# Kernel optimization log

Hardware: AMD Instinct MI355X
Metric: run time of the kernel (lower is better)

## Reference

```python
import jax, jax.numpy as jnp
import numpy as np

K = 5          # number of neighbors (init kwarg k)
EPS = 1e-7     # init kwarg eps
_D2_MIN = 1e-12  # clamp squared distances so sqrt is grad-safe on the diagonal


def _cdist(A):
    # Euclidean pairwise distances, [N, N]
    sq = jnp.sum(A * A, axis=1)
    d2 = sq[:, None] + sq[None, :] - 2.0 * (A @ A.T)
    return jnp.sqrt(jnp.maximum(d2, _D2_MIN))


def setup_inputs() -> dict:
    key = jax.random.key(0)
    k1, k2 = jax.random.split(key)
    X = jax.random.normal(k1, (8192, 512), dtype=jnp.float32)
    Z = jax.random.normal(k2, (8192, 128), dtype=jnp.float32)
    return {"X": X, "Z": Z}


def reference(X, Z):
    # 0.98-quantile of row norms (torch.quantile default = linear interpolation)
    normA1 = jnp.quantile(jnp.sqrt(jnp.sum(X ** 2, axis=1)), 0.98)
    normA2 = jnp.quantile(jnp.sqrt(jnp.sum(Z ** 2, axis=1)), 0.98)

    # --- neighbor mask + LID on X ---
    x_dist = (_cdist(X) + EPS) / normA1                      # [N, N]
    neg_vals, idx = jax.lax.top_k(-x_dist, K + 1)            # k+1 smallest, ascending
    values = -neg_vals[:, 1:]                                # drop self, [N, K]
    nn_mask = idx[:, 1:]                                     # neighbor indices, [N, K]
    lid_X = jnp.sum(jnp.log10(values) - jnp.log10(values[:, -1:]), axis=1)  # [N]

    # --- gather same neighbors in Z-space ---
    z_dist = (_cdist(Z) + EPS) / normA2                      # [N, N]
    extracted = jnp.take_along_axis(z_dist, nn_mask, axis=1)  # [N, K]
    norm_v = jnp.max(extracted, axis=1, keepdims=True)        # [N, 1]
    lid_Z = jnp.sum(jnp.log10(extracted) - jnp.log10(norm_v), axis=1)  # [N]

    N = X.shape[0]
    diff = K / (lid_X + EPS) - K / (lid_Z + EPS)
    return jnp.sum(jnp.square(diff)) / (N * K * K)
```

## Files before the change

kernel.cpp:

```cpp
#include <hip/hip_runtime.h>
#include <hip/hip_bf16.h>
#include <math.h>


#define NROWS 8192
#define DX 512
#define DZ 128
#define KNN 5
#define NSTRIP 4
#define SSPAN (NROWS / NSTRIP)
#define BM 128
#define BN 256
#define NJT (SSPAN / BN)
#define NCAND (NSTRIP * KNN)
#define QSCALE 30.0f

typedef int i32x4 __attribute__((ext_vector_type(4)));
typedef int i32x16 __attribute__((ext_vector_type(16)));

__device__ __forceinline__ bool ilexless(int d1, int i1, int d2, int i2) {
  return (d1 < d2) || (d1 == d2 && i1 < i2);
}
__device__ __forceinline__ bool flexless(float d1, int i1, float d2, int i2) {
  return (d1 < d2) || (d1 == d2 && i1 < i2);
}

__device__ __forceinline__ void ins5k(int k, int* md) {
  if (k >= md[4]) return;
  int nk = k;
#pragma unroll
  for (int p = 0; p < 5; ++p) {
    const bool sw = nk < md[p];
    const int tk = sw ? md[p] : nk;
    md[p] = sw ? nk : md[p];
    nk = tk;
  }
}
__device__ __forceinline__ void ins6k(int k, int* md) {
  if (k >= md[5]) return;
  int nk = k;
#pragma unroll
  for (int p = 0; p < 6; ++p) {
    const bool sw = nk < md[p];
    const int tk = sw ? md[p] : nk;
    md[p] = sw ? nk : md[p];
    nk = tk;
  }
}
__device__ __forceinline__ void ins8i(int d, int i, int* md, int* mi) {
  if (!ilexless(d, i, md[7], mi[7])) return;
  int nd = d, ni = i;
#pragma unroll
  for (int p = 0; p < 8; ++p) {
    const bool sw = ilexless(nd, ni, md[p], mi[p]);
    const int td = sw ? md[p] : nd; const int ti = sw ? mi[p] : ni;
    md[p] = sw ? nd : md[p]; mi[p] = sw ? ni : mi[p];
    nd = td; ni = ti;
  }
}
__device__ __forceinline__ void ins5f(float d, int i, float* md, int* mi) {
  if (!flexless(d, i, md[4], mi[4])) return;
  float nd = d; int ni = i;
#pragma unroll
  for (int p = 0; p < 5; ++p) {
    const bool sw = flexless(nd, ni, md[p], mi[p]);
    const float td = sw ? md[p] : nd; const int ti = sw ? mi[p] : ni;
    md[p] = sw ? nd : md[p]; mi[p] = sw ? ni : mi[p];
    nd = td; ni = ti;
  }
}

__device__ __forceinline__ void gload_lds16(const void* g, void* l) {
  __builtin_amdgcn_global_load_lds((const __attribute__((address_space(1))) void*)g,
                                   (__attribute__((address_space(3))) void*)l,
                                   16, 0, 0);
}

__global__ __launch_bounds__(256) void prep_kernel(const float* __restrict__ X,
                                                   const float* __restrict__ Z,
                                                   signed char* __restrict__ Xq,
                                                   float* __restrict__ sqx,
                                                   int* __restrict__ sqq,
                                                   float* __restrict__ sqz) {
  const int b = blockIdx.x;
  const int w = threadIdx.x >> 6;
  const int lane = threadIdx.x & 63;
  if (b < NROWS / 4) {
    const int row = (b << 2) + w;
    const float* p = X + (size_t)row * DX + lane * 8;
    const float4 v0 = *(const float4*)(p);
    const float4 v1 = *(const float4*)(p + 4);
    float xs[8] = {v0.x, v0.y, v0.z, v0.w, v1.x, v1.y, v1.z, v1.w};
    float s = 0.f;
    int q[8];
    int si = 0;
#pragma unroll
    for (int j = 0; j < 8; ++j) {
      s = fmaf(xs[j], xs[j], s);
      q[j] = (int)rintf(fminf(fmaxf(xs[j] * QSCALE, -127.f), 127.f));
      si += q[j] * q[j];
    }
    const int b0 = (q[0] & 255) | ((q[1] & 255) << 8) | ((q[2] & 255) << 16) | ((q[3] & 255) << 24);
    const int b1 = (q[4] & 255) | ((q[5] & 255) << 8) | ((q[6] & 255) << 16) | ((q[7] & 255) << 24);
    *(int2*)(Xq + (size_t)row * DX + lane * 8) = make_int2(b0, b1);
#pragma unroll
    for (int off = 32; off > 0; off >>= 1) {
      s += __shfl_down(s, off, 64);
      si += __shfl_down(si, off, 64);
    }
    if (lane == 0) { sqx[row] = s; sqq[row] = si; }
  } else {
    const int row = ((b - NROWS / 4) << 2) + w;
    const float* p = Z + (size_t)row * DZ;
    const float a = p[lane];
    const float c = p[64 + lane];
    float s = fmaf(a, a, c * c);
#pragma unroll
    for (int off = 32; off > 0; off >>= 1) s += __shfl_down(s, off, 64);
    if (lane == 0) sqz[row] = s;
  }
}

__global__ __launch_bounds__(1024) void stats_kernel(const int* __restrict__ sqq,
                                                     float* __restrict__ stats) {
  __shared__ double sw[16], sw2[16];
  const int t = threadIdx.x;
  double s = 0.0, s2 = 0.0;
  for (int i = t; i < NROWS; i += 1024) {
    const double v = (double)sqq[i];
    s += v; s2 += v * v;
  }
#pragma unroll
  for (int off = 32; off > 0; off >>= 1) {
    s += __shfl_down(s, off, 64);
    s2 += __shfl_down(s2, off, 64);
  }
  if ((t & 63) == 0) { sw[t >> 6] = s; sw2[t >> 6] = s2; }
  __syncthreads();
  if (t < 16) {
    double v = sw[t], v2 = sw2[t];
#pragma unroll
    for (int off = 8; off > 0; off >>= 1) {
      v += __shfl_down(v, off, 64);
      v2 += __shfl_down(v2, off, 64);
    }
    if (t == 0) {
      const double mu = v / (double)NROWS;
      stats[0] = (float)mu;
      stats[1] = (float)(v2 / (double)NROWS - mu * mu);
    }
  }
}

__global__ __launch_bounds__(1024, 1) void knn_i8_kernel(const signed char* __restrict__ Xq,
                                                         const int* __restrict__ sqq,
                                                         const float* __restrict__ stats,
                                                         int* __restrict__ cand_i,
                                                         int* __restrict__ cand_m) {
  extern __shared__ __align__(16) char lds[];
  char* ldsA = lds;
  char* ldsBb = lds + 65536;
  int* qs = (int*)(lds + 114688);

  const int bid = blockIdx.x;
  const int strip = bid & 3;
  const int rowchunk = bid >> 2;
  const int I0 = rowchunk * BM;
  const int J0 = strip * SSPAN;

  const int t = threadIdx.x;
  const int w = t >> 6;
  const int lane = t & 63;
  const int l31 = lane & 31, lh5 = lane >> 5;
  const int cq = w & 3, rh = w >> 2;

  const float mu = stats[0];
  const float var = stats[1];
  const int lr = (rh << 5) + l31;
  const int tau = (int)(mu - 2.2f * sqrtf(var + (mu * 0.0078125f) * (float)sqq[I0 + lr]));
  const int taubase = tau - 262144;

  const char* Aaddr = ldsA + (lh5 << 11) + (lr << 4);
  const int bcol = ((cq << 6) + l31) << 4;
  const char* Ba0 = ldsBb + (lh5 << 12) + bcol;
  const char* Ba1 = Ba0 + 16384;
  const char* Ba2 = Ba0 + 32768;
  char* Da0 = ldsBb + ((w >> 2) << 12) + ((w & 3) << 10);
  char* Da1 = Da0 + 16384;
  char* Da2 = Da0 + 32768;
  const signed char* sj = Xq + (size_t)(J0 + ((w & 3) << 6) + lane) * DX + ((w >> 2) << 4);
  const int* qw = qs + (cq << 6) + (lh5 << 2);
  int colj = J0 + (cq << 6) + (lh5 << 2);

#pragma unroll
  for (int i = 0; i < 4; ++i) {
    const int idx = (w << 2) + i;
    const int g = idx >> 1, half = idx & 1;
    gload_lds16(Xq + (size_t)(I0 + half * 64 + lane) * DX + (g << 4),
                ldsA + g * 2048 + half * 1024);
  }
  if (w < 8)
    gload_lds16((const char*)(sqq + J0) + (w << 10) + (lane << 4),
                (char*)qs + (w << 10));
  gload_lds16(sj, Da0);
  gload_lds16(sj + 64, Da1);

  const i32x16 z16 = {0, 0, 0, 0, 0, 0, 0, 0, 0, 0, 0, 0, 0, 0, 0, 0};
  i32x16 acc[2];
  int md6[6];
#pragma unroll
  for (int q = 0; q < 6; ++q) md6[q] = 0x7fffffff;

  for (int jt = 0; jt < NJT; ++jt) {
    const signed char* sj2 = sj + BN * DX;
#pragma unroll
    for (int kb = 0; kb < 8; ++kb) {
      if (kb < 7 || jt < NJT - 1) {
        asm volatile("s_waitcnt vmcnt(1)" ::: "memory");
      } else {
        asm volatile("s_waitcnt vmcnt(0)" ::: "memory");
      }
      __builtin_amdgcn_s_barrier();
      __builtin_amdgcn_sched_barrier(0);
      char* D = (kb % 3 == 1) ? Da0 : (kb % 3 == 2) ? Da1 : Da2;
      if (kb <= 5) {
        gload_lds16(sj + (kb + 2) * 64, D);
      } else if (jt < NJT - 1) {
        gload_lds16(sj2 + (kb - 6) * 64, D);
      }
      if (kb == 0) { acc[0] = z16; acc[1] = z16; }
      const char* B = (kb % 3 == 0) ? Ba0 : (kb % 3 == 1) ? Ba1 : Ba2;
#pragma unroll
      for (int ktl = 0; ktl < 2; ++ktl) {
        const i32x4 ap0 = *(const i32x4*)(B + ktl * 8192);
        const i32x4 ap1 = *(const i32x4*)(B + ktl * 8192 + 512);
        const i32x4 bp = *(const i32x4*)(Aaddr + kb * 8192 + ktl * 4096);
        acc[0] = __builtin_amdgcn_mfma_i32_32x32x32_i8(ap0, bp, acc[0], 0, 0, 0);
        acc[1] = __builtin_amdgcn_mfma_i32_32x32x32_i8(ap1, bp, acc[1], 0, 0, 0);
      }
      if (kb == 7) {
#pragma unroll
        for (int n = 0; n < 2; ++n) {
          const i32x4 q0 = *(const i32x4*)(qw + n * 32);
          const i32x4 q1 = *(const i32x4*)(qw + n * 32 + 8);
          const i32x4 q2 = *(const i32x4*)(qw + n * 32 + 16);
          const i32x4 q3 = *(const i32x4*)(qw + n * 32 + 24);
#pragma unroll
          for (int reg = 0; reg < 16; ++reg) {
            const int qv = (reg < 4) ? q0[reg & 3] : (reg < 8) ? q1[reg & 3]
                         : (reg < 12) ? q2[reg & 3] : q3[reg & 3];
            const int d = qv - 2 * acc[n][reg];
            if (d < tau) {
              const int cconst = (reg & 3) + ((reg >> 2) << 3);
              const int col = colj + n * 32 + cconst;
              const int v = max(d - taubase, 0);
              ins6k((v << 13) | col, md6);
            }
          }
        }
      }
    }
    { const char* tmp = Ba2; Ba2 = Ba1; Ba1 = Ba0; Ba0 = tmp; }
    { char* tmp = Da2; Da2 = Da1; Da1 = Da0; Da0 = tmp; }
    sj = sj2; qw += BN; colj += BN;
  }

  __syncthreads();

  int* pm = (int*)ldsBb;
  {
    const int sub = (cq << 1) | lh5;
#pragma unroll
    for (int q = 0; q < 6; ++q) pm[(lr * 8 + sub) * 6 + q] = md6[q];
  }
  __syncthreads();
  if (t < BM) {
    int md[5];
#pragma unroll
    for (int q = 0; q < 5; ++q) md[q] = 0x7fffffff;
    const int rgg = I0 + t;
    for (int c = 0; c < 8; ++c)
#pragma unroll
      for (int q = 0; q < 6; ++q) {
        const int key = pm[(t * 8 + c) * 6 + q];
        if ((key & 8191) != rgg) ins5k(key, md);
      }
    const size_t base = (size_t)(I0 + t) * NCAND + strip * KNN;
#pragma unroll
    for (int q = 0; q < 5; ++q) {
      cand_m[base + q] = md[q];
      cand_i[base + q] = (md[q] == 0x7fffffff) ? 0x7fffffff : (md[q] & 8191);
    }
  }
}

__global__ __launch_bounds__(256) void rerank_kernel(const float* __restrict__ X,
                                                     const float* __restrict__ Z,
                                                     const float* __restrict__ sqx,
                                                     const float* __restrict__ sqz,
                                                     const int* __restrict__ cand_i,
                                                     const int* __restrict__ cand_m,
                                                     float* __restrict__ row_out) {
  __shared__ float xrow[4][DX];
  const int w = threadIdx.x >> 6;
  const int lane = threadIdx.x & 63;
  const int row = (blockIdx.x << 2) + w;

  const float* xp = X + (size_t)row * DX + lane * 8;
  *(float4*)&xrow[w][lane * 8] = *(const float4*)(xp);
  *(float4*)&xrow[w][lane * 8 + 4] = *(const float4*)(xp + 4);

  int cm = 0x7fffffff, ci = 0x7fffffff;
  if (lane < NCAND) {
    cm = cand_m[(size_t)row * NCAND + lane];
    ci = cand_i[(size_t)row * NCAND + lane];
  }
  __syncthreads();

  int m8[8], i8v[8];
#pragma unroll
  for (int q = 0; q < 8; ++q) { m8[q] = 0x7fffffff; i8v[q] = 0x7fffffff; }
#pragma unroll
  for (int c = 0; c < NCAND; ++c) {
    const int dm = __shfl(cm, c, 64);
    const int di = __shfl(ci, c, 64);
    ins8i(dm, di, m8, i8v);
  }

  const int cgrp = lane >> 3, sgi = lane & 7;
  int j = (cgrp == 0) ? i8v[0] : (cgrp == 1) ? i8v[1] : (cgrp == 2) ? i8v[2] :
          (cgrp == 3) ? i8v[3] : (cgrp == 4) ? i8v[4] : (cgrp == 5) ? i8v[5] :
          (cgrp == 6) ? i8v[6] : i8v[7];
  if ((unsigned)j >= NROWS) j = 0;
  const float* yp = X + (size_t)j * DX + sgi * 64;
  const float* xq_ = &xrow[w][sgi * 64];
  float dot = 0.f;
#pragma unroll 8
  for (int k = 0; k < 64; k += 4) {
    const float4 xv = *(const float4*)(xq_ + k);
    const float4 yv = *(const float4*)(yp + k);
    dot = fmaf(xv.x, yv.x, dot);
    dot = fmaf(xv.y, yv.y, dot);
    dot = fmaf(xv.z, yv.z, dot);
    dot = fmaf(xv.w, yv.w, dot);
  }
  dot += __shfl_xor(dot, 1, 64);
  dot += __shfl_xor(dot, 2, 64);
  dot += __shfl_xor(dot, 4, 64);
  const float d2 = sqx[row] + sqx[j] - 2.f * dot;

  float fd[5]; int fi[5];
#pragma unroll
  for (int q = 0; q < 5; ++q) { fd[q] = INFINITY; fi[q] = 0x7fffffff; }
#pragma unroll
  for (int cc = 0; cc < 8; ++cc) {
    const float dd = __shfl(d2, cc * 8, 64);
    if (lane == 0) ins5f(dd, i8v[cc], fd, fi);
  }
  float lidX = 0.f;
  if (lane == 0) {
    const float v4 = sqrtf(fmaxf(fd[4], 1e-12f)) + 1e-7f;
    const float l4 = log10f(v4);
#pragma unroll
    for (int q = 0; q < 5; ++q) {
      const float v = sqrtf(fmaxf(fd[q], 1e-12f)) + 1e-7f;
      lidX += log10f(v) - l4;
    }
  }
  int nb[5];
#pragma unroll
  for (int q = 0; q < 5; ++q) {
    nb[q] = __shfl(fi[q], 0, 64);
    if ((unsigned)nb[q] >= NROWS) nb[q] = 0;
  }

  const float zi0 = Z[(size_t)row * DZ + lane];
  const float zi1 = Z[(size_t)row * DZ + 64 + lane];
  float ez[5];
#pragma unroll
  for (int q = 0; q < 5; ++q) {
    const float* zn = Z + (size_t)nb[q] * DZ;
    float p = fmaf(zi0, zn[lane], zi1 * zn[64 + lane]);
#pragma unroll
    for (int off = 32; off > 0; off >>= 1) p += __shfl_down(p, off, 64);
    ez[q] = p;
  }
  if (lane == 0) {
    const float sqzr = sqz[row];
    float e[5];
    float mx = -INFINITY;
#pragma unroll
    for (int q = 0; q < 5; ++q) {
      const float d2z = sqzr + sqz[nb[q]] - 2.f * ez[q];
      e[q] = sqrtf(fmaxf(d2z, 1e-12f)) + 1e-7f;
      mx = fmaxf(mx, e[q]);
    }
    const float lmx = log10f(mx);
    float lidZ = 0.f;
#pragma unroll
    for (int q = 0; q < 5; ++q) lidZ += log10f(e[q]) - lmx;
    const float diff = 5.0f / (lidX + 1e-7f) - 5.0f / (lidZ + 1e-7f);
    row_out[row] = diff * diff;
  }
}

__global__ __launch_bounds__(1024) void reduce_kernel(const float* __restrict__ row_out,
                                                      float* __restrict__ out) {
  __shared__ float sw[16];
  const int t = threadIdx.x;
  float s = 0.f;
  for (int i = t; i < NROWS; i += 1024) s += row_out[i];
#pragma unroll
  for (int off = 32; off > 0; off >>= 1) s += __shfl_down(s, off, 64);
  if ((t & 63) == 0) sw[t >> 6] = s;
  __syncthreads();
  if (t < 16) {
    float v = sw[t];
#pragma unroll
    for (int off = 8; off > 0; off >>= 1) v += __shfl_down(v, off, 64);
    if (t == 0) out[0] = v * (1.0f / (8192.0f * 25.0f));
  }
}

extern "C" void kernel_launch(void* const* d_in, const int* in_sizes, int n_in,
                              void* d_out, int out_size, void* d_ws, size_t ws_size,
                              hipStream_t stream) {
  const float* X = (const float*)d_in[0];
  const float* Z = (const float*)d_in[1];
  float* out = (float*)d_out;

  char* wb = (char*)d_ws;
  signed char* Xq = (signed char*)wb;
  float* sqx = (float*)(wb + (size_t)NROWS * DX);
  int* sqq = (int*)(sqx + NROWS);
  float* sqz = (float*)(sqq + NROWS);
  int* cand_i = (int*)(sqz + NROWS);
  int* cand_m = cand_i + (size_t)NROWS * NCAND;
  float* row_out = (float*)(cand_m + (size_t)NROWS * NCAND);
  float* stats = row_out + NROWS;

  prep_kernel<<<NROWS / 2, 256, 0, stream>>>(X, Z, Xq, sqx, sqq, sqz);
  stats_kernel<<<1, 1024, 0, stream>>>(sqq, stats);
  knn_i8_kernel<<<NSTRIP * (NROWS / BM), 1024, 122880, stream>>>(Xq, sqq, stats, cand_i, cand_m);
  rerank_kernel<<<NROWS / 4, 256, 0, stream>>>(X, Z, sqx, sqz, cand_i, cand_m, row_out);
  reduce_kernel<<<1, 1024, 0, stream>>>(row_out, out);
}
```

Measured before the change: 117.3 us.

## Restructure B-tile pipeline to four LDS buffers with two k-blocks per barrier

The int8 kNN GEMM's B operand moves from a triple-buffered ring (one k-block per barrier, vmcnt(1)) to a four-buffer layout. Each barrier stage now loads and computes two k-blocks, waiting with vmcnt(0). This halves the number of workgroup barriers per tile and removes the rotating buffer pointers, at the cost of 16 KB more LDS and a shallower prefetch lead relative to compute.

```diff
diff --git a/kernel.cpp b/kernel.cpp
--- a/kernel.cpp
+++ b/kernel.cpp
@@ -160,7 +160,7 @@
   extern __shared__ __align__(16) char lds[];
   char* ldsA = lds;
   char* ldsBb = lds + 65536;
-  int* qs = (int*)(lds + 114688);
+  int* qs = (int*)(lds + 131072);
 
   const int bid = blockIdx.x;
   const int strip = bid & 3;
@@ -181,13 +181,8 @@
   const int taubase = tau - 262144;
 
   const char* Aaddr = ldsA + (lh5 << 11) + (lr << 4);
-  const int bcol = ((cq << 6) + l31) << 4;
-  const char* Ba0 = ldsBb + (lh5 << 12) + bcol;
-  const char* Ba1 = Ba0 + 16384;
-  const char* Ba2 = Ba0 + 32768;
-  char* Da0 = ldsBb + ((w >> 2) << 12) + ((w & 3) << 10);
-  char* Da1 = Da0 + 16384;
-  char* Da2 = Da0 + 32768;
+  const char* Bbase = ldsBb + (lh5 << 12) + (((cq << 6) + l31) << 4);
+  char* Dst = ldsBb + ((w >> 2) << 12) + ((w & 3) << 10);
   const signed char* sj = Xq + (size_t)(J0 + ((w & 3) << 6) + lane) * DX + ((w >> 2) << 4);
   const int* qw = qs + (cq << 6) + (lh5 << 2);
   int colj = J0 + (cq << 6) + (lh5 << 2);
@@ -202,8 +197,8 @@
   if (w < 8)
     gload_lds16((const char*)(sqq + J0) + (w << 10) + (lane << 4),
                 (char*)qs + (w << 10));
-  gload_lds16(sj, Da0);
-  gload_lds16(sj + 64, Da1);
+  gload_lds16(sj, Dst);
+  gload_lds16(sj + 64, Dst + 16384);
 
   const i32x16 z16 = {0, 0, 0, 0, 0, 0, 0, 0, 0, 0, 0, 0, 0, 0, 0, 0};
   i32x16 acc[2];
@@ -214,31 +209,32 @@
   for (int jt = 0; jt < NJT; ++jt) {
     const signed char* sj2 = sj + BN * DX;
 #pragma unroll
-    for (int kb = 0; kb < 8; ++kb) {
-      if (kb < 7 || jt < NJT - 1) {
-        asm volatile("s_waitcnt vmcnt(1)" ::: "memory");
-      } else {
-        asm volatile("s_waitcnt vmcnt(0)" ::: "memory");
-      }
+    for (int pp = 0; pp < 4; ++pp) {
+      asm volatile("s_waitcnt vmcnt(0)" ::: "memory");
       __builtin_amdgcn_s_barrier();
       __builtin_amdgcn_sched_barrier(0);
-      char* D = (kb % 3 == 1) ? Da0 : (kb % 3 == 2) ? Da1 : Da2;
-      if (kb <= 5) {
-        gload_lds16(sj + (kb + 2) * 64, D);
+      if (pp < 3) {
+        gload_lds16(sj + (2 * pp + 2) * 64, Dst + (((2 * pp + 2) & 3) << 14));
+        gload_lds16(sj + (2 * pp + 3) * 64, Dst + (((2 * pp + 3) & 3) << 14));
       } else if (jt < NJT - 1) {
-        gload_lds16(sj2 + (kb - 6) * 64, D);
+        gload_lds16(sj2, Dst);
+        gload_lds16(sj2 + 64, Dst + 16384);
       }
-      if (kb == 0) { acc[0] = z16; acc[1] = z16; }
-      const char* B = (kb % 3 == 0) ? Ba0 : (kb % 3 == 1) ? Ba1 : Ba2;
-#pragma unroll
-      for (int ktl = 0; ktl < 2; ++ktl) {
-        const i32x4 ap0 = *(const i32x4*)(B + ktl * 8192);
-        const i32x4 ap1 = *(const i32x4*)(B + ktl * 8192 + 512);
-        const i32x4 bp = *(const i32x4*)(Aaddr + kb * 8192 + ktl * 4096);
-        acc[0] = __builtin_amdgcn_mfma_i32_32x32x32_i8(ap0, bp, acc[0], 0, 0, 0);
-        acc[1] = __builtin_amdgcn_mfma_i32_32x32x32_i8(ap1, bp, acc[1], 0, 0, 0);
+      if (pp == 0) { acc[0] = z16; acc[1] = z16; }
+#pragma unroll
+      for (int half = 0; half < 2; ++half) {
+        const int kb = 2 * pp + half;
+        const char* B = Bbase + ((kb & 3) << 14);
+#pragma unroll
+        for (int ktl = 0; ktl < 2; ++ktl) {
+          const i32x4 ap0 = *(const i32x4*)(B + ktl * 8192);
+          const i32x4 ap1 = *(const i32x4*)(B + ktl * 8192 + 512);
+          const i32x4 bp = *(const i32x4*)(Aaddr + kb * 8192 + ktl * 4096);
+          acc[0] = __builtin_amdgcn_mfma_i32_32x32x32_i8(ap0, bp, acc[0], 0, 0, 0);
+          acc[1] = __builtin_amdgcn_mfma_i32_32x32x32_i8(ap1, bp, acc[1], 0, 0, 0);
+        }
       }
-      if (kb == 7) {
+      if (pp == 3) {
 #pragma unroll
         for (int n = 0; n < 2; ++n) {
           const i32x4 q0 = *(const i32x4*)(qw + n * 32);
@@ -260,8 +256,6 @@
         }
       }
     }
-    { const char* tmp = Ba2; Ba2 = Ba1; Ba1 = Ba0; Ba0 = tmp; }
-    { char* tmp = Da2; Da2 = Da1; Da1 = Da0; Da0 = tmp; }
     sj = sj2; qw += BN; colj += BN;
   }
 
@@ -441,7 +435,7 @@
 
   prep_kernel<<<NROWS / 2, 256, 0, stream>>>(X, Z, Xq, sqx, sqq, sqz);
   stats_kernel<<<1, 1024, 0, stream>>>(sqq, stats);
-  knn_i8_kernel<<<NSTRIP * (NROWS / BM), 1024, 122880, stream>>>(Xq, sqq, stats, cand_i, cand_m);
+  knn_i8_kernel<<<NSTRIP * (NROWS / BM), 1024, 139264, stream>>>(Xq, sqq, stats, cand_i, cand_m);
   rerank_kernel<<<NROWS / 4, 256, 0, stream>>>(X, Z, sqx, sqz, cand_i, cand_m, row_out);
   reduce_kernel<<<1, 1024, 0, stream>>>(row_out, out);
 }
```

New measurement: 123.9 us. +5.7%, slower.
